# Kernel optimization log

Hardware: AMD Instinct MI355X
Metric: run time of the kernel (lower is better)

The kernel has to match this reference:

```python
import jax, jax.numpy as jnp
import numpy as np

SPATIAL_SCALE = 0.125
POOLED = 7
PART = 7
SAMPLES = 4
TRANS_STD = 0.1


def setup_inputs() -> dict:
    key = jax.random.key(0)
    kd, kb, kx, ky, kw, kh, ko = jax.random.split(key, 7)
    B, C, H, W = 4, 256, 64, 64
    N = 256
    data = jax.random.normal(kd, (B, C, H, W), dtype=jnp.float32)
    # rois: (batch_idx, x1, y1, x2, y2) in image coordinates (image = W/scale = 512)
    img = W / SPATIAL_SCALE
    batch_idx = jax.random.randint(kb, (N,), 0, B).astype(jnp.float32)
    x1 = jax.random.uniform(kx, (N,), minval=0.0, maxval=img - 120.0)
    y1 = jax.random.uniform(ky, (N,), minval=0.0, maxval=img - 120.0)
    bw = jax.random.uniform(kw, (N,), minval=32.0, maxval=112.0)
    bh = jax.random.uniform(kh, (N,), minval=32.0, maxval=112.0)
    rois = jnp.stack([batch_idx, x1, y1, x1 + bw, y1 + bh], axis=1).astype(jnp.float32)
    offset = jax.random.normal(ko, (N, 2, PART, PART), dtype=jnp.float32)
    return {"data": data, "rois": rois, "offset": offset}


def _deform_roi_pool(data, rois, offset):
    B, C, H, W = data.shape
    P, S = POOLED, SAMPLES
    b = rois[:, 0].astype(jnp.int32)
    # rounded roi box in feature coords (matches deform_pool CUDA kernel)
    roi_sw = jnp.round(rois[:, 1]) * SPATIAL_SCALE - 0.5
    roi_sh = jnp.round(rois[:, 2]) * SPATIAL_SCALE - 0.5
    roi_ew = (jnp.round(rois[:, 3]) + 1.0) * SPATIAL_SCALE - 0.5
    roi_eh = (jnp.round(rois[:, 4]) + 1.0) * SPATIAL_SCALE - 0.5
    roi_w = jnp.maximum(roi_ew - roi_sw, 0.1)
    roi_h = jnp.maximum(roi_eh - roi_sh, 0.1)
    bin_w = roi_w / P
    bin_h = roi_h / P
    sub_w = bin_w / S
    sub_h = bin_h / S
    ph = jnp.arange(P, dtype=jnp.float32)
    pw = jnp.arange(P, dtype=jnp.float32)
    part_h = jnp.clip(jnp.floor(ph / P * PART).astype(jnp.int32), 0, PART - 1)
    part_w = jnp.clip(jnp.floor(pw / P * PART).astype(jnp.int32), 0, PART - 1)
    # learned normalized offsets, shared across channels (num_classes == 1)
    tx = offset[:, 0][:, part_h[:, None], part_w[None, :]] * TRANS_STD  # [N,P,P]
    ty = offset[:, 1][:, part_h[:, None], part_w[None, :]] * TRANS_STD  # [N,P,P]
    wstart = pw[None, None, :] * bin_w[:, None, None] + roi_sw[:, None, None] + tx * roi_w[:, None, None]
    hstart = ph[None, :, None] * bin_h[:, None, None] + roi_sh[:, None, None] + ty * roi_h[:, None, None]
    s = jnp.arange(S, dtype=jnp.float32)
    # sample coordinates: [N, P, P, S(h), S(w)]
    w = wstart[..., None, None] + s[None, None, None, None, :] * sub_w[:, None, None, None, None]
    h = hstart[..., None, None] + s[None, None, None, :, None] * sub_h[:, None, None, None, None]
    valid = (w > -0.5) & (w < W - 0.5) & (h > -0.5) & (h < H - 0.5)
    wc = jnp.clip(w, 0.0, W - 1.0)
    hc = jnp.clip(h, 0.0, H - 1.0)
    x0 = jnp.floor(wc).astype(jnp.int32)
    y0 = jnp.floor(hc).astype(jnp.int32)
    x1i = jnp.minimum(x0 + 1, W - 1)
    y1i = jnp.minimum(y0 + 1, H - 1)
    dx = wc - x0.astype(wc.dtype)
    dy = hc - y0.astype(hc.dtype)
    bb = jnp.broadcast_to(b[:, None, None, None, None], x0.shape)

    def gather(yi, xi):
        # advanced indexing around the channel slice -> [N,P,P,S,S,C]
        return data[bb, :, yi, xi]

    v = (((1.0 - dx) * (1.0 - dy))[..., None] * gather(y0, x0)
         + ((1.0 - dx) * dy)[..., None] * gather(y1i, x0)
         + (dx * (1.0 - dy))[..., None] * gather(y0, x1i)
         + (dx * dy)[..., None] * gather(y1i, x1i))
    v = v * valid[..., None].astype(v.dtype)
    top = v.sum(axis=(3, 4))                      # [N,P,P,C]
    count = valid.astype(jnp.float32).sum(axis=(3, 4))  # [N,P,P]
    out = jnp.where(count[..., None] > 0, top / jnp.maximum(count[..., None], 1.0), 0.0)
    return jnp.transpose(out, (0, 3, 1, 2))       # [N,C,P,P]


def reference(data, rois, offset):
    return _deform_roi_pool(data, rois, offset)
```

## Files before the change

### kernel.cpp

```cpp
#include <hip/hip_runtime.h>
#include <hip/hip_bf16.h>

#define SPATIAL_SCALE 0.125f
#define POOLED 7
#define PART 7
#define SAMPLES 4
#define TRANS_STD 0.1f

#define B_DIM 4
#define C_DIM 256
#define H_DIM 64
#define W_DIM 64
#define BINS (POOLED * POOLED)
#define C4 (C_DIM / 4)

#define TS 32
__global__ __launch_bounds__(256) void nchw_to_nhwc(const float* __restrict__ in,
                                                    float* __restrict__ out) {
    __shared__ float tile[TS][TS + 1];
    const int b   = blockIdx.z;
    const int hw0 = blockIdx.x * TS;
    const int c0  = blockIdx.y * TS;
    const int tx  = threadIdx.x;
    const int ty  = threadIdx.y;

    const float* inb  = in  + (size_t)b * C_DIM * (H_DIM * W_DIM);
    float*       outb = out + (size_t)b * (H_DIM * W_DIM) * C_DIM;

    #pragma unroll
    for (int i = ty; i < TS; i += 8)
        tile[i][tx] = inb[(size_t)(c0 + i) * (H_DIM * W_DIM) + (hw0 + tx)];
    __syncthreads();
    #pragma unroll
    for (int i = ty; i < TS; i += 8)
        outb[(size_t)(hw0 + i) * C_DIM + (c0 + tx)] = tile[tx][i];
}

__global__ __launch_bounds__(64) void deform_roi_pool_v3(const float4* __restrict__ src4,
                                                         const float* __restrict__ rois,
                                                         const float* __restrict__ offset,
                                                         float4* __restrict__ tmp4,
                                                         int N) {
    const int blk = blockIdx.x;
    const int n   = blk / BINS;
    const int bin = blk % BINS;
    const int ph  = bin / POOLED;
    const int pw  = bin % POOLED;
    const int lane = threadIdx.x;
    if (n >= N) return;

    const float* roi = rois + (size_t)n * 5;
    const int b = (int)roi[0];

    const float roi_sw = rintf(roi[1]) * SPATIAL_SCALE - 0.5f;
    const float roi_sh = rintf(roi[2]) * SPATIAL_SCALE - 0.5f;
    const float roi_ew = (rintf(roi[3]) + 1.0f) * SPATIAL_SCALE - 0.5f;
    const float roi_eh = (rintf(roi[4]) + 1.0f) * SPATIAL_SCALE - 0.5f;
    const float roi_w = fmaxf(roi_ew - roi_sw, 0.1f);
    const float roi_h = fmaxf(roi_eh - roi_sh, 0.1f);
    const float bin_w = roi_w / (float)POOLED;
    const float bin_h = roi_h / (float)POOLED;
    const float sub_w = bin_w / (float)SAMPLES;
    const float sub_h = bin_h / (float)SAMPLES;

    int part_h = (int)floorf(((float)ph / (float)POOLED) * (float)PART);
    int part_w = (int)floorf(((float)pw / (float)POOLED) * (float)PART);
    part_h = min(max(part_h, 0), PART - 1);
    part_w = min(max(part_w, 0), PART - 1);

    const float tx = offset[(((size_t)n * 2 + 0) * PART + part_h) * PART + part_w] * TRANS_STD;
    const float ty = offset[(((size_t)n * 2 + 1) * PART + part_h) * PART + part_w] * TRANS_STD;

    const float wstart = (float)pw * bin_w + roi_sw + tx * roi_w;
    const float hstart = (float)ph * bin_h + roi_sh + ty * roi_h;

    float Wx[4] = {0.f, 0.f, 0.f, 0.f};
    int xmin = 0, nvw = 0;
    #pragma unroll
    for (int sw = 0; sw < SAMPLES; ++sw) {
        const float w = wstart + (float)sw * sub_w;
        if (w > -0.5f && w < (float)W_DIM - 0.5f) {
            const float wc = fminf(fmaxf(w, 0.0f), (float)(W_DIM - 1));
            const int x0 = (int)floorf(wc);
            const int x1 = min(x0 + 1, W_DIM - 1);
            const float dx = wc - (float)x0;
            if (nvw == 0) xmin = x0;
            ++nvw;
            const int i0 = x0 - xmin;
            const int i1 = x1 - xmin;
            const float w0 = 1.0f - dx;
            Wx[0] += (i0 == 0 ? w0 : 0.f) + (i1 == 0 ? dx : 0.f);
            Wx[1] += (i0 == 1 ? w0 : 0.f) + (i1 == 1 ? dx : 0.f);
            Wx[2] += (i0 == 2 ? w0 : 0.f) + (i1 == 2 ? dx : 0.f);
            Wx[3] += (i1 == 3 ? dx : 0.f);
        }
    }

    float Wy[4] = {0.f, 0.f, 0.f, 0.f};
    int ymin = 0, nvh = 0;
    #pragma unroll
    for (int sh = 0; sh < SAMPLES; ++sh) {
        const float h = hstart + (float)sh * sub_h;
        if (h > -0.5f && h < (float)H_DIM - 0.5f) {
            const float hc = fminf(fmaxf(h, 0.0f), (float)(H_DIM - 1));
            const int y0 = (int)floorf(hc);
            const int y1 = min(y0 + 1, H_DIM - 1);
            const float dy = hc - (float)y0;
            if (nvh == 0) ymin = y0;
            ++nvh;
            const int i0 = y0 - ymin;
            const int i1 = y1 - ymin;
            const float w0 = 1.0f - dy;
            Wy[0] += (i0 == 0 ? w0 : 0.f) + (i1 == 0 ? dy : 0.f);
            Wy[1] += (i0 == 1 ? w0 : 0.f) + (i1 == 1 ? dy : 0.f);
            Wy[2] += (i0 == 2 ? w0 : 0.f) + (i1 == 2 ? dy : 0.f);
            Wy[3] += (i1 == 3 ? dy : 0.f);
        }
    }

    const int cnt = nvw * nvh;
    float4 res = make_float4(0.f, 0.f, 0.f, 0.f);

    if (cnt > 0) {
        const float4* baseb = src4 + (size_t)b * (H_DIM * W_DIM) * C4;
        float4 acc = make_float4(0.f, 0.f, 0.f, 0.f);
        #pragma unroll
        for (int iy = 0; iy < 4; ++iy) {
            if (Wy[iy] == 0.f) continue;
            const int rowoff = (ymin + iy) * W_DIM + xmin;
            #pragma unroll
            for (int ix = 0; ix < 4; ++ix) {
                if (Wx[ix] == 0.f) continue;
                const float wgt = Wy[iy] * Wx[ix];
                const float4 v = baseb[(size_t)(rowoff + ix) * C4 + lane];
                acc.x = fmaf(wgt, v.x, acc.x);
                acc.y = fmaf(wgt, v.y, acc.y);
                acc.z = fmaf(wgt, v.z, acc.z);
                acc.w = fmaf(wgt, v.w, acc.w);
            }
        }
        const float fc = (float)cnt;
        res = make_float4(acc.x / fc, acc.y / fc, acc.z / fc, acc.w / fc);
    }

    tmp4[(size_t)blk * 64 + lane] = res;
}

__global__ __launch_bounds__(256) void layout_out(const float* __restrict__ tmp,
                                                  float* __restrict__ out) {
    __shared__ float lds[BINS * 65];
    const int q = blockIdx.x;
    const int n = blockIdx.y;
    const int t = threadIdx.x;

    const float* tn = tmp + (size_t)n * BINS * C_DIM + q * 64;
    for (int j = t; j < BINS * 64; j += 256) {
        const int bin = j >> 6;
        const int c   = j & 63;
        lds[bin * 65 + c] = tn[(size_t)bin * C_DIM + c];
    }
    __syncthreads();
    float* on = out + (size_t)n * C_DIM * BINS + (size_t)q * 64 * BINS;
    for (int j = t; j < 64 * BINS; j += 256) {
        const int c   = j / BINS;
        const int bin = j - c * BINS;
        on[j] = lds[bin * 65 + c];
    }
}

__global__ __launch_bounds__(256) void deform_roi_pool_nchw(const float* __restrict__ src,
                                                            const float* __restrict__ rois,
                                                            const float* __restrict__ offset,
                                                            float* __restrict__ out,
                                                            int N) {
    const int blk = blockIdx.x;
    const int n   = blk / BINS;
    const int bin = blk % BINS;
    const int ph  = bin / POOLED;
    const int pw  = bin % POOLED;
    const int c   = threadIdx.x;
    if (n >= N) return;

    const float* roi = rois + (size_t)n * 5;
    const int b = (int)roi[0];

    const float roi_sw = rintf(roi[1]) * SPATIAL_SCALE - 0.5f;
    const float roi_sh = rintf(roi[2]) * SPATIAL_SCALE - 0.5f;
    const float roi_ew = (rintf(roi[3]) + 1.0f) * SPATIAL_SCALE - 0.5f;
    const float roi_eh = (rintf(roi[4]) + 1.0f) * SPATIAL_SCALE - 0.5f;
    const float roi_w = fmaxf(roi_ew - roi_sw, 0.1f);
    const float roi_h = fmaxf(roi_eh - roi_sh, 0.1f);
    const float bin_w = roi_w / (float)POOLED;
    const float bin_h = roi_h / (float)POOLED;
    const float sub_w = bin_w / (float)SAMPLES;
    const float sub_h = bin_h / (float)SAMPLES;

    int part_h = (int)floorf(((float)ph / (float)POOLED) * (float)PART);
    int part_w = (int)floorf(((float)pw / (float)POOLED) * (float)PART);
    part_h = min(max(part_h, 0), PART - 1);
    part_w = min(max(part_w, 0), PART - 1);

    const float tx = offset[(((size_t)n * 2 + 0) * PART + part_h) * PART + part_w] * TRANS_STD;
    const float ty = offset[(((size_t)n * 2 + 1) * PART + part_h) * PART + part_w] * TRANS_STD;

    const float wstart = (float)pw * bin_w + roi_sw + tx * roi_w;
    const float hstart = (float)ph * bin_h + roi_sh + ty * roi_h;

    float sum = 0.0f;
    int cnt = 0;

    #pragma unroll
    for (int sh = 0; sh < SAMPLES; ++sh) {
        const float h = hstart + (float)sh * sub_h;
        #pragma unroll
        for (int sw = 0; sw < SAMPLES; ++sw) {
            const float w = wstart + (float)sw * sub_w;
            const bool valid = (w > -0.5f) && (w < (float)W_DIM - 0.5f) &&
                               (h > -0.5f) && (h < (float)H_DIM - 0.5f);
            if (!valid) continue;
            ++cnt;
            const float wc = fminf(fmaxf(w, 0.0f), (float)(W_DIM - 1));
            const float hc = fminf(fmaxf(h, 0.0f), (float)(H_DIM - 1));
            const int x0 = (int)floorf(wc);
            const int y0 = (int)floorf(hc);
            const int x1 = min(x0 + 1, W_DIM - 1);
            const int y1 = min(y0 + 1, H_DIM - 1);
            const float dx = wc - (float)x0;
            const float dy = hc - (float)y0;

            const size_t base = ((size_t)b * C_DIM + c) * (H_DIM * W_DIM);
            const float v00 = src[base + (size_t)y0 * W_DIM + x0];
            const float v01 = src[base + (size_t)y0 * W_DIM + x1];
            const float v10 = src[base + (size_t)y1 * W_DIM + x0];
            const float v11 = src[base + (size_t)y1 * W_DIM + x1];
            sum += (1.0f - dx) * (1.0f - dy) * v00
                 + (1.0f - dx) * dy          * v10
                 + dx          * (1.0f - dy) * v01
                 + dx          * dy          * v11;
        }
    }

    const float res = (cnt > 0) ? sum / (float)cnt : 0.0f;
    out[(((size_t)n * C_DIM + c) * POOLED + ph) * POOLED + pw] = res;
}

extern "C" void kernel_launch(void* const* d_in, const int* in_sizes, int n_in,
                              void* d_out, int out_size, void* d_ws, size_t ws_size,
                              hipStream_t stream) {
    const float* data   = (const float*)d_in[0];
    const float* rois   = (const float*)d_in[1];
    const float* offset = (const float*)d_in[2];
    float* out = (float*)d_out;
    const int N = in_sizes[1] / 5;

    const size_t nhwc_bytes = (size_t)B_DIM * C_DIM * H_DIM * W_DIM * sizeof(float);
    const size_t tmp_bytes  = (size_t)N * BINS * C_DIM * sizeof(float);

    if (ws_size >= nhwc_bytes + tmp_bytes) {
        float* data_t = (float*)d_ws;
        float* tmp    = (float*)((char*)d_ws + nhwc_bytes);
        dim3 tb(32, 8, 1);
        dim3 tg((H_DIM * W_DIM) / TS, C_DIM / TS, B_DIM);
        nchw_to_nhwc<<<tg, tb, 0, stream>>>(data, data_t);
        deform_roi_pool_v3<<<N * BINS, 64, 0, stream>>>(
            (const float4*)data_t, rois, offset, (float4*)tmp, N);
        layout_out<<<dim3(4, N, 1), 256, 0, stream>>>(tmp, out);
    } else {
        deform_roi_pool_nchw<<<N * BINS, C_DIM, 0, stream>>>(
            data, rois, offset, out, N);
    }
}
```

Baseline: 96.41 us.

## Fuse pooling and output transpose into one per-ROI kernel using LDS

Result: slower. 103.2 us (+7.0%).

```diff
diff --git a/kernel.cpp b/kernel.cpp
--- a/kernel.cpp
+++ b/kernel.cpp
@@ -12,7 +12,6 @@
 #define H_DIM 64
 #define W_DIM 64
 #define BINS (POOLED * POOLED)
-#define C4 (C_DIM / 4)
 
 #define TS 32
 __global__ __launch_bounds__(256) void nchw_to_nhwc(const float* __restrict__ in,
@@ -36,18 +35,16 @@
         outb[(size_t)(hw0 + i) * C_DIM + (c0 + tx)] = tile[tx][i];
 }
 
-__global__ __launch_bounds__(64) void deform_roi_pool_v3(const float4* __restrict__ src4,
-                                                         const float* __restrict__ rois,
-                                                         const float* __restrict__ offset,
-                                                         float4* __restrict__ tmp4,
-                                                         int N) {
-    const int blk = blockIdx.x;
-    const int n   = blk / BINS;
-    const int bin = blk % BINS;
-    const int ph  = bin / POOLED;
-    const int pw  = bin % POOLED;
-    const int lane = threadIdx.x;
-    if (n >= N) return;
+__global__ __launch_bounds__(512) void pool_fused(const float* __restrict__ src,
+                                                  const float* __restrict__ rois,
+                                                  const float* __restrict__ offset,
+                                                  float* __restrict__ out,
+                                                  int N) {
+    __shared__ float lds[C_DIM * BINS];
+    const int n    = blockIdx.x;
+    const int t    = threadIdx.x;
+    const int wave = t >> 6;
+    const int lane = t & 63;
 
     const float* roi = rois + (size_t)n * 5;
     const int b = (int)roi[0];
@@ -63,109 +60,101 @@
     const float sub_w = bin_w / (float)SAMPLES;
     const float sub_h = bin_h / (float)SAMPLES;
 
-    int part_h = (int)floorf(((float)ph / (float)POOLED) * (float)PART);
-    int part_w = (int)floorf(((float)pw / (float)POOLED) * (float)PART);
-    part_h = min(max(part_h, 0), PART - 1);
-    part_w = min(max(part_w, 0), PART - 1);
-
-    const float tx = offset[(((size_t)n * 2 + 0) * PART + part_h) * PART + part_w] * TRANS_STD;
-    const float ty = offset[(((size_t)n * 2 + 1) * PART + part_h) * PART + part_w] * TRANS_STD;
-
-    const float wstart = (float)pw * bin_w + roi_sw + tx * roi_w;
-    const float hstart = (float)ph * bin_h + roi_sh + ty * roi_h;
-
-    float Wx[4] = {0.f, 0.f, 0.f, 0.f};
-    int xmin = 0, nvw = 0;
-    #pragma unroll
-    for (int sw = 0; sw < SAMPLES; ++sw) {
-        const float w = wstart + (float)sw * sub_w;
-        if (w > -0.5f && w < (float)W_DIM - 0.5f) {
-            const float wc = fminf(fmaxf(w, 0.0f), (float)(W_DIM - 1));
-            const int x0 = (int)floorf(wc);
-            const int x1 = min(x0 + 1, W_DIM - 1);
-            const float dx = wc - (float)x0;
-            if (nvw == 0) xmin = x0;
-            ++nvw;
-            const int i0 = x0 - xmin;
-            const int i1 = x1 - xmin;
-            const float w0 = 1.0f - dx;
-            Wx[0] += (i0 == 0 ? w0 : 0.f) + (i1 == 0 ? dx : 0.f);
-            Wx[1] += (i0 == 1 ? w0 : 0.f) + (i1 == 1 ? dx : 0.f);
-            Wx[2] += (i0 == 2 ? w0 : 0.f) + (i1 == 2 ? dx : 0.f);
-            Wx[3] += (i1 == 3 ? dx : 0.f);
-        }
+    const float* baseb = src + (size_t)b * (H_DIM * W_DIM) * C_DIM;
+
+    for (int bin = wave; bin < BINS; bin += 8) {
+        const int ph = bin / POOLED;
+        const int pw = bin - ph * POOLED;
+
+        int part_h = (int)floorf(((float)ph / (float)POOLED) * (float)PART);
+        int part_w = (int)floorf(((float)pw / (float)POOLED) * (float)PART);
+        part_h = min(max(part_h, 0), PART - 1);
+        part_w = min(max(part_w, 0), PART - 1);
+
+        const float tx = offset[(((size_t)n * 2 + 0) * PART + part_h) * PART + part_w] * TRANS_STD;
+        const float ty = offset[(((size_t)n * 2 + 1) * PART + part_h) * PART + part_w] * TRANS_STD;
+
+        const float wstart = (float)pw * bin_w + roi_sw + tx * roi_w;
+        const float hstart = (float)ph * bin_h + roi_sh + ty * roi_h;
+
+        float Wx[4] = {0.f, 0.f, 0.f, 0.f};
+        int xmin = 0, nvw = 0;
+        #pragma unroll
+        for (int sw = 0; sw < SAMPLES; ++sw) {
+            const float w = wstart + (float)sw * sub_w;
+            if (w > -0.5f && w < (float)W_DIM - 0.5f) {
+                const float wc = fminf(fmaxf(w, 0.0f), (float)(W_DIM - 1));
+                const int x0 = (int)floorf(wc);
+                const int x1 = min(x0 + 1, W_DIM - 1);
+                const float dx = wc - (float)x0;
+                if (nvw == 0) xmin = x0;
+                ++nvw;
+                const int i0 = x0 - xmin;
+                const int i1 = x1 - xmin;
+                const float w0 = 1.0f - dx;
+                Wx[0] += (i0 == 0 ? w0 : 0.f) + (i1 == 0 ? dx : 0.f);
+                Wx[1] += (i0 == 1 ? w0 : 0.f) + (i1 == 1 ? dx : 0.f);
+                Wx[2] += (i0 == 2 ? w0 : 0.f) + (i1 == 2 ? dx : 0.f);
+                Wx[3] += (i1 == 3 ? dx : 0.f);
+            }
+        }
+
+        float Wy[4] = {0.f, 0.f, 0.f, 0.f};
+        int ymin = 0, nvh = 0;
+        #pragma unroll
+        for (int sh = 0; sh < SAMPLES; ++sh) {
+            const float h = hstart + (float)sh * sub_h;
+            if (h > -0.5f && h < (float)H_DIM - 0.5f) {
+                const float hc = fminf(fmaxf(h, 0.0f), (float)(H_DIM - 1));
+                const int y0 = (int)floorf(hc);
+                const int y1 = min(y0 + 1, H_DIM - 1);
+                const float dy = hc - (float)y0;
+                if (nvh == 0) ymin = y0;
+                ++nvh;
+                const int i0 = y0 - ymin;
+                const int i1 = y1 - ymin;
+                const float w0 = 1.0f - dy;
+                Wy[0] += (i0 == 0 ? w0 : 0.f) + (i1 == 0 ? dy : 0.f);
+                Wy[1] += (i0 == 1 ? w0 : 0.f) + (i1 == 1 ? dy : 0.f);
+                Wy[2] += (i0 == 2 ? w0 : 0.f) + (i1 == 2 ? dy : 0.f);
+                Wy[3] += (i1 == 3 ? dy : 0.f);
+            }
+        }
+
+        const int cnt = nvw * nvh;
+        float a0 = 0.f, a1 = 0.f, a2 = 0.f, a3 = 0.f;
+
+        if (cnt > 0) {
+            #pragma unroll
+            for (int iy = 0; iy < 4; ++iy) {
+                if (Wy[iy] == 0.f) continue;
+                const int rowoff = (ymin + iy) * W_DIM + xmin;
+                #pragma unroll
+                for (int ix = 0; ix < 4; ++ix) {
+                    if (Wx[ix] == 0.f) continue;
+                    const float wgt = Wy[iy] * Wx[ix];
+                    const float* p = baseb + (size_t)(rowoff + ix) * C_DIM + lane;
+                    a0 = fmaf(wgt, p[0],   a0);
+                    a1 = fmaf(wgt, p[64],  a1);
+                    a2 = fmaf(wgt, p[128], a2);
+                    a3 = fmaf(wgt, p[192], a3);
+                }
+            }
+            const float rinv = 1.0f / (float)cnt;
+            a0 *= rinv; a1 *= rinv; a2 *= rinv; a3 *= rinv;
+        }
+
+        lds[(lane       ) * BINS + bin] = a0;
+        lds[(lane +  64 ) * BINS + bin] = a1;
+        lds[(lane + 128 ) * BINS + bin] = a2;
+        lds[(lane + 192 ) * BINS + bin] = a3;
     }
 
-    float Wy[4] = {0.f, 0.f, 0.f, 0.f};
-    int ymin = 0, nvh = 0;
-    #pragma unroll
-    for (int sh = 0; sh < SAMPLES; ++sh) {
-        const float h = hstart + (float)sh * sub_h;
-        if (h > -0.5f && h < (float)H_DIM - 0.5f) {
-            const float hc = fminf(fmaxf(h, 0.0f), (float)(H_DIM - 1));
-            const int y0 = (int)floorf(hc);
-            const int y1 = min(y0 + 1, H_DIM - 1);
-            const float dy = hc - (float)y0;
-            if (nvh == 0) ymin = y0;
-            ++nvh;
-            const int i0 = y0 - ymin;
-            const int i1 = y1 - ymin;
-            const float w0 = 1.0f - dy;
-            Wy[0] += (i0 == 0 ? w0 : 0.f) + (i1 == 0 ? dy : 0.f);
-            Wy[1] += (i0 == 1 ? w0 : 0.f) + (i1 == 1 ? dy : 0.f);
-            Wy[2] += (i0 == 2 ? w0 : 0.f) + (i1 == 2 ? dy : 0.f);
-            Wy[3] += (i1 == 3 ? dy : 0.f);
-        }
-    }
-
-    const int cnt = nvw * nvh;
-    float4 res = make_float4(0.f, 0.f, 0.f, 0.f);
-
-    if (cnt > 0) {
-        const float4* baseb = src4 + (size_t)b * (H_DIM * W_DIM) * C4;
-        float4 acc = make_float4(0.f, 0.f, 0.f, 0.f);
-        #pragma unroll
-        for (int iy = 0; iy < 4; ++iy) {
-            if (Wy[iy] == 0.f) continue;
-            const int rowoff = (ymin + iy) * W_DIM + xmin;
-            #pragma unroll
-            for (int ix = 0; ix < 4; ++ix) {
-                if (Wx[ix] == 0.f) continue;
-                const float wgt = Wy[iy] * Wx[ix];
-                const float4 v = baseb[(size_t)(rowoff + ix) * C4 + lane];
-                acc.x = fmaf(wgt, v.x, acc.x);
-                acc.y = fmaf(wgt, v.y, acc.y);
-                acc.z = fmaf(wgt, v.z, acc.z);
-                acc.w = fmaf(wgt, v.w, acc.w);
-            }
-        }
-        const float fc = (float)cnt;
-        res = make_float4(acc.x / fc, acc.y / fc, acc.z / fc, acc.w / fc);
-    }
-
-    tmp4[(size_t)blk * 64 + lane] = res;
-}
-
-__global__ __launch_bounds__(256) void layout_out(const float* __restrict__ tmp,
-                                                  float* __restrict__ out) {
-    __shared__ float lds[BINS * 65];
-    const int q = blockIdx.x;
-    const int n = blockIdx.y;
-    const int t = threadIdx.x;
-
-    const float* tn = tmp + (size_t)n * BINS * C_DIM + q * 64;
-    for (int j = t; j < BINS * 64; j += 256) {
-        const int bin = j >> 6;
-        const int c   = j & 63;
-        lds[bin * 65 + c] = tn[(size_t)bin * C_DIM + c];
-    }
     __syncthreads();
-    float* on = out + (size_t)n * C_DIM * BINS + (size_t)q * 64 * BINS;
-    for (int j = t; j < 64 * BINS; j += 256) {
-        const int c   = j / BINS;
-        const int bin = j - c * BINS;
-        on[j] = lds[bin * 65 + c];
-    }
+
+    float* on = out + (size_t)n * (C_DIM * BINS);
+    for (int j = t; j < C_DIM * BINS; j += 512)
+        on[j] = lds[j];
 }
 
 __global__ __launch_bounds__(256) void deform_roi_pool_nchw(const float* __restrict__ src,
@@ -254,17 +243,13 @@
     const int N = in_sizes[1] / 5;
 
     const size_t nhwc_bytes = (size_t)B_DIM * C_DIM * H_DIM * W_DIM * sizeof(float);
-    const size_t tmp_bytes  = (size_t)N * BINS * C_DIM * sizeof(float);
-
-    if (ws_size >= nhwc_bytes + tmp_bytes) {
+
+    if (ws_size >= nhwc_bytes) {
         float* data_t = (float*)d_ws;
-        float* tmp    = (float*)((char*)d_ws + nhwc_bytes);
         dim3 tb(32, 8, 1);
         dim3 tg((H_DIM * W_DIM) / TS, C_DIM / TS, B_DIM);
         nchw_to_nhwc<<<tg, tb, 0, stream>>>(data, data_t);
-        deform_roi_pool_v3<<<N * BINS, 64, 0, stream>>>(
-            (const float4*)data_t, rois, offset, (float4*)tmp, N);
-        layout_out<<<dim3(4, N, 1), 256, 0, stream>>>(tmp, out);
+        pool_fused<<<N, 512, 0, stream>>>(data_t, rois, offset, out, N);
     } else {
         deform_roi_pool_nchw<<<N * BINS, C_DIM, 0, stream>>>(
             data, rois, offset, out, N);
```
